# Kernel tuning notes

Hardware: AMD Instinct MI355X
Metric: run time of the kernel (lower is better)

Reference implementation:

```python
import jax, jax.numpy as jnp
import numpy as np

B, T, D_IN, H, E = 256, 512, 256, 256, 96  # batch, enc seq, input_size, hidden_size, num_embeddings


def setup_inputs() -> dict:
    key = jax.random.key(0)
    ks = jax.random.split(key, 12)
    s = 0.05
    return {
        "prev_h": jax.random.normal(ks[0], (B, H), jnp.float32),
        "prev_c": jax.random.normal(ks[1], (B, H), jnp.float32),
        "batch_H": jax.random.normal(ks[2], (B, T, D_IN), jnp.float32),
        "char_onehots": jax.random.uniform(ks[3], (B, E), jnp.float32),
        "W_i2h": jax.random.normal(ks[4], (H, D_IN), jnp.float32) * s,
        "W_h2h": jax.random.normal(ks[5], (H, H), jnp.float32) * s,
        "b_h2h": jax.random.normal(ks[6], (H,), jnp.float32) * s,
        "W_score": jax.random.normal(ks[7], (1, H), jnp.float32) * s,
        "W_ih": jax.random.normal(ks[8], (4 * H, D_IN + E), jnp.float32) * s,
        "W_hh": jax.random.normal(ks[9], (4 * H, H), jnp.float32) * s,
        "b_ih": jax.random.normal(ks[10], (4 * H,), jnp.float32) * s,
        "b_hh": jax.random.normal(ks[11], (4 * H,), jnp.float32) * s,
    }


def reference(prev_h, prev_c, batch_H, char_onehots,
              W_i2h, W_h2h, b_h2h, W_score, W_ih, W_hh, b_ih, b_hh):
    # additive attention over encoder features
    proj = jnp.einsum('btd,hd->bth', batch_H, W_i2h)          # [B,T,H]
    hid = prev_h @ W_h2h.T + b_h2h                             # [B,H]
    e = jnp.einsum('bth,oh->bto', jnp.tanh(proj + hid[:, None, :]), W_score)  # [B,T,1]
    alpha = jax.nn.softmax(e, axis=1)                          # [B,T,1]
    context = jnp.einsum('bt,btd->bd', alpha[..., 0], batch_H) # [B,D_IN]
    x = jnp.concatenate([context, char_onehots], axis=1)       # [B,D_IN+E]
    # LSTM cell step (PyTorch gate order: i, f, g, o)
    gates = x @ W_ih.T + b_ih + prev_h @ W_hh.T + b_hh         # [B,4H]
    i, f, g, o = jnp.split(gates, 4, axis=1)
    c_new = jax.nn.sigmoid(f) * prev_c + jax.nn.sigmoid(i) * jnp.tanh(g)
    h_new = jax.nn.sigmoid(o) * jnp.tanh(c_new)
    return (h_new, c_new, jnp.swapaxes(alpha, 1, 2))           # alpha -> [B,1,T]
```

## Files before the change

kernel.cpp:

```cpp
#include <hip/hip_runtime.h>

typedef __attribute__((ext_vector_type(8))) short short8;
typedef __attribute__((ext_vector_type(4))) float f32x4;

#define KPAD 40

#define WS_HID    0u
#define WS_P      262144u
#define WS_Z      786432u
#define WS_CTX    794624u
#define WS_CTXP   1056768u
#define WS_WBF    3153920u

__device__ __forceinline__ unsigned f2bfu(float f) {
    union { float f; unsigned u; } v; v.f = f;
    return (v.u + 0x7FFFu + ((v.u >> 16) & 1u)) >> 16;
}
__device__ __forceinline__ float bf2f(short s) {
    union { float f; unsigned u; } v; v.u = ((unsigned)(unsigned short)s) << 16;
    return v.f;
}
__device__ __forceinline__ float tanh_fast(float x) {
    float e2 = __expf(2.f * x);
    return 1.f - 2.f * __builtin_amdgcn_rcpf(e2 + 1.f);
}
__device__ __forceinline__ float sigmoid_fast(float x) {
    return __builtin_amdgcn_rcpf(1.f + __expf(-x));
}
__device__ __forceinline__ int4 pack8(float4 x0, float4 x1) {
    int4 q;
    q.x = (int)((f2bfu(x0.y) << 16) | f2bfu(x0.x));
    q.y = (int)((f2bfu(x0.w) << 16) | f2bfu(x0.z));
    q.z = (int)((f2bfu(x1.y) << 16) | f2bfu(x1.x));
    q.w = (int)((f2bfu(x1.w) << 16) | f2bfu(x1.z));
    return q;
}

__global__ __launch_bounds__(256) void k_prep(
    const float* __restrict__ prev_h, const float* __restrict__ W_i2h,
    const float* __restrict__ W_h2h, const float* __restrict__ b_h2h,
    float* __restrict__ hid, short* __restrict__ Wbf)
{
    int bid = blockIdx.x, tid = threadIdx.x;
    if (bid < 256) {
        __shared__ float ph[256];
        ph[tid] = prev_h[bid * 256 + tid];
        __syncthreads();
        float acc = b_h2h[tid];
        const float4* w = (const float4*)(W_h2h + tid * 256);
        #pragma unroll 8
        for (int k4 = 0; k4 < 64; ++k4) {
            float4 ww = w[k4];
            acc += ww.x * ph[k4*4+0] + ww.y * ph[k4*4+1] + ww.z * ph[k4*4+2] + ww.w * ph[k4*4+3];
        }
        hid[bid * 256 + tid] = acc;
    } else {
        int idx = (bid - 256) * 256 + tid;
        int kc = idx / (256 * KPAD);
        int rem = idx % (256 * KPAD);
        int n = rem / KPAD, kk = rem % KPAD;
        float v = (kk < 32) ? W_i2h[n * 256 + kc * 32 + kk] : 0.f;
        Wbf[idx] = (short)f2bfu(v);
    }
}

__global__ __launch_bounds__(256, 2) void k_escore_ctx(
    const float* __restrict__ BH, const short* __restrict__ Wbf,
    const float* __restrict__ hid, const float* __restrict__ Wsc,
    float* __restrict__ p_out, float* __restrict__ zbuf, float* __restrict__ ctxp)
{
    __shared__ char smem[81920];
    short* Al = (short*)smem;
    short* Bl = (short*)(smem + 40960);
    float* eps = (float*)(smem + 40960);
    float* pl  = (float*)(smem + 41984);
    float* r8  = (float*)(smem + 42240);

    const int tid = threadIdx.x;
    const int lane = tid & 63;
    const int w = tid >> 6;
    const int l15 = lane & 15, lg = lane >> 4;
    const int bt0 = blockIdx.x * 64;
    const int b = bt0 >> 9;
    const int c = (bt0 >> 6) & 7;

    const int arow = tid >> 2, akg = tid & 3;
    const float* asrc = BH + (size_t)(bt0 + arow) * 256 + akg * 8;

    f32x4 acc[4][4];
    #pragma unroll
    for (int i = 0; i < 4; i++)
        #pragma unroll
        for (int j = 0; j < 4; j++) acc[i][j] = (f32x4){0.f, 0.f, 0.f, 0.f};

    auto stage = [&](int kc) {
        float4 x0 = *(const float4*)(asrc + kc * 32);
        float4 x1 = *(const float4*)(asrc + kc * 32 + 4);
        *(int4*)&Al[kc * 2560 + arow * KPAD + akg * 8] = pack8(x0, x1);
        const int4* bs = (const int4*)(Wbf + (size_t)(kc * 256 + tid) * KPAD);
        int4* bd = (int4*)&Bl[(kc & 1) * 10240 + tid * KPAD];
        #pragma unroll
        for (int i = 0; i < 5; i++) bd[i] = bs[i];
    };

    stage(0);
    __syncthreads();

    for (int ks = 0; ks < 8; ++ks) {
        short8 af[4], bf_[4];
        #pragma unroll
        for (int rf = 0; rf < 4; rf++)
            af[rf] = *(const short8*)&Al[ks * 2560 + (rf * 16 + l15) * KPAD + lg * 8];
        #pragma unroll
        for (int cf = 0; cf < 4; cf++)
            bf_[cf] = *(const short8*)&Bl[(ks & 1) * 10240 + (w * 64 + cf * 16 + l15) * KPAD + lg * 8];
        if (ks < 7) stage(ks + 1);
        #pragma unroll
        for (int rf = 0; rf < 4; rf++)
            #pragma unroll
            for (int cf = 0; cf < 4; cf++)
                acc[rf][cf] = __builtin_amdgcn_mfma_f32_16x16x32_bf16(af[rf], bf_[cf], acc[rf][cf], 0, 0, 0);
        __syncthreads();
    }

    float esum[4][4];
    #pragma unroll
    for (int rf = 0; rf < 4; rf++)
        #pragma unroll
        for (int r = 0; r < 4; r++) esum[rf][r] = 0.f;

    #pragma unroll
    for (int cf = 0; cf < 4; cf++) {
        int col = w * 64 + cf * 16 + l15;
        float wsv = Wsc[col];
        float hd = hid[b * 256 + col];
        #pragma unroll
        for (int rf = 0; rf < 4; rf++)
            #pragma unroll
            for (int r = 0; r < 4; r++)
                esum[rf][r] += wsv * tanh_fast(acc[rf][cf][r] + hd);
    }
    #pragma unroll
    for (int rf = 0; rf < 4; rf++)
        #pragma unroll
        for (int r = 0; r < 4; r++) {
            float s = esum[rf][r];
            s += __shfl_xor(s, 1); s += __shfl_xor(s, 2);
            s += __shfl_xor(s, 4); s += __shfl_xor(s, 8);
            esum[rf][r] = s;
        }
    if (l15 == 0) {
        #pragma unroll
        for (int rf = 0; rf < 4; rf++)
            #pragma unroll
            for (int r = 0; r < 4; r++)
                eps[w * 64 + rf * 16 + lg * 4 + r] = esum[rf][r];
    }
    __syncthreads();

    if (tid < 64) {
        float e = eps[tid] + eps[64 + tid] + eps[128 + tid] + eps[192 + tid];
        float p = __expf(e);
        p_out[bt0 + tid] = p;
        pl[tid] = p;
        float z = p;
        z += __shfl_xor(z, 1); z += __shfl_xor(z, 2); z += __shfl_xor(z, 4);
        z += __shfl_xor(z, 8); z += __shfl_xor(z, 16); z += __shfl_xor(z, 32);
        if (tid == 0) zbuf[blockIdx.x] = z;
    }
    __syncthreads();

    {
        int tg = tid & 7, dg = tid >> 3;
        int d0 = dg * 8;
        int kc = d0 >> 5, dd = d0 & 31;
        float a8[8] = {0.f,0.f,0.f,0.f,0.f,0.f,0.f,0.f};
        #pragma unroll
        for (int tt = 0; tt < 8; ++tt) {
            int t = tt * 8 + tg;
            short8 v = *(const short8*)&Al[kc * 2560 + t * KPAD + dd];
            float pv = pl[t];
            #pragma unroll
            for (int j = 0; j < 8; ++j) a8[j] += pv * bf2f(v[j]);
        }
        #pragma unroll
        for (int j = 0; j < 8; ++j) r8[tg * 256 + d0 + j] = a8[j];
    }
    __syncthreads();
    {
        float s = 0.f;
        #pragma unroll
        for (int g = 0; g < 8; ++g) s += r8[g * 256 + tid];
        ctxp[((size_t)(c * 256 + b)) * 256 + tid] = s;
    }
}

__global__ __launch_bounds__(256) void k_finalize(
    const float* __restrict__ p, const float* __restrict__ zbuf,
    const float* __restrict__ ctxp, float* __restrict__ alpha, float* __restrict__ ctx)
{
    int b = blockIdx.x, t = threadIdx.x;
    float Z = 0.f;
    #pragma unroll
    for (int cc = 0; cc < 8; ++cc) Z += zbuf[b * 8 + cc];
    float inv = 1.f / Z;
    alpha[b * 512 + t] = p[b * 512 + t] * inv;
    alpha[b * 512 + 256 + t] = p[b * 512 + 256 + t] * inv;
    float s = 0.f;
    #pragma unroll
    for (int cc = 0; cc < 8; ++cc) s += ctxp[((size_t)(cc * 256 + b)) * 256 + t];
    ctx[b * 256 + t] = s * inv;
}

__global__ __launch_bounds__(256) void k_gates_lstm(
    const float* __restrict__ ctx, const float* __restrict__ onehot,
    const float* __restrict__ prev_h, const float* __restrict__ W_ih,
    const float* __restrict__ W_hh, const float* __restrict__ b_ih,
    const float* __restrict__ b_hh, const float* __restrict__ prev_c,
    float* __restrict__ out)
{
    __shared__ char smem[20800];
    short* AlB = (short*)smem;
    short* BlB = (short*)smem + 5120;
    const int tid = threadIdx.x;
    const int lane = tid & 63;
    const int w = tid >> 6;
    const int l15 = lane & 15, lg = lane >> 4;
    const int rb = blockIdx.x * 64;
    const int hb = blockIdx.y;

    f32x4 acc[4];
    #pragma unroll
    for (int j = 0; j < 4; j++) acc[j] = (f32x4){0.f, 0.f, 0.f, 0.f};

    const int arow = tid >> 2, akg = tid & 3;
    const int rg = rb + arow;
    const int bn = tid >> 2, bq = tid & 3;
    const int np_ = hb * 64 + bn, hh_ = np_ >> 2, gg_ = np_ & 3;
    const float* wih_row = W_ih + (size_t)(gg_ * 256 + hh_) * 352;
    const float* whh_row = W_hh + (size_t)(gg_ * 256 + hh_) * 256;

    auto stageAB = [&](int kc, int bu) {
        int k0 = kc * 32 + akg * 8;
        const float4* pa;
        if (k0 < 256)      pa = (const float4*)(ctx    + rg * 256 + k0);
        else if (k0 < 352) pa = (const float4*)(onehot + rg * 96  + (k0 - 256));
        else               pa = (const float4*)(prev_h + rg * 256 + (k0 - 352));
        float4 x0 = pa[0], x1 = pa[1];
        *(int4*)&AlB[bu * 2560 + arow * KPAD + akg * 8] = pack8(x0, x1);
        int kb = kc * 32 + bq * 8;
        const float* pb = (kb < 352) ? (wih_row + kb) : (whh_row + (kb - 352));
        float4 y0 = *(const float4*)pb, y1 = *(const float4*)(pb + 4);
        *(int4*)&BlB[bu * 2560 + bn * KPAD + bq * 8] = pack8(y0, y1);
    };

    stageAB(0, 0);
    __syncthreads();

    for (int kc = 0; kc < 19; ++kc) {
        int cur = kc & 1;
        short8 af = *(const short8*)&AlB[cur * 2560 + (w * 16 + l15) * KPAD + lg * 8];
        short8 bf_[4];
        #pragma unroll
        for (int cf = 0; cf < 4; cf++)
            bf_[cf] = *(const short8*)&BlB[cur * 2560 + (cf * 16 + l15) * KPAD + lg * 8];
        if (kc < 18) stageAB(kc + 1, cur ^ 1);
        #pragma unroll
        for (int cf = 0; cf < 4; cf++)
            acc[cf] = __builtin_amdgcn_mfma_f32_16x16x32_bf16(af, bf_[cf], acc[cf], 0, 0, 0);
        __syncthreads();
    }

    float* Gt = (float*)smem;
    #pragma unroll
    for (int cf = 0; cf < 4; cf++) {
        int col = cf * 16 + l15;
        int np = hb * 64 + col;
        int hg = np >> 2, g = np & 3;
        float bias = b_ih[g * 256 + hg] + b_hh[g * 256 + hg];
        #pragma unroll
        for (int r = 0; r < 4; r++)
            Gt[(w * 16 + lg * 4 + r) * 65 + col] = acc[cf][r] + bias;
    }
    __syncthreads();

    #pragma unroll
    for (int it = 0; it < 4; ++it) {
        int elem = it * 256 + tid;
        int row = elem >> 4, hl = elem & 15;
        float gi = Gt[row * 65 + hl * 4 + 0];
        float gf = Gt[row * 65 + hl * 4 + 1];
        float gg = Gt[row * 65 + hl * 4 + 2];
        float go = Gt[row * 65 + hl * 4 + 3];
        int bg = rb + row, hglob = hb * 16 + hl;
        float cv = sigmoid_fast(gf) * prev_c[bg * 256 + hglob] + sigmoid_fast(gi) * tanh_fast(gg);
        out[bg * 256 + hglob] = sigmoid_fast(go) * tanh_fast(cv);
        out[65536 + bg * 256 + hglob] = cv;
    }
}

extern "C" void kernel_launch(void* const* d_in, const int* in_sizes, int n_in,
                              void* d_out, int out_size, void* d_ws, size_t ws_size,
                              hipStream_t stream) {
    (void)in_sizes; (void)n_in; (void)out_size; (void)ws_size;
    const float* prev_h  = (const float*)d_in[0];
    const float* prev_c  = (const float*)d_in[1];
    const float* batch_H = (const float*)d_in[2];
    const float* onehot  = (const float*)d_in[3];
    const float* W_i2h   = (const float*)d_in[4];
    const float* W_h2h   = (const float*)d_in[5];
    const float* b_h2h   = (const float*)d_in[6];
    const float* W_score = (const float*)d_in[7];
    const float* W_ih    = (const float*)d_in[8];
    const float* W_hh    = (const float*)d_in[9];
    const float* b_ih    = (const float*)d_in[10];
    const float* b_hh    = (const float*)d_in[11];

    char* ws = (char*)d_ws;
    float* hid   = (float*)(ws + WS_HID);
    float* p     = (float*)(ws + WS_P);
    float* zbuf  = (float*)(ws + WS_Z);
    float* ctx   = (float*)(ws + WS_CTX);
    float* ctxp  = (float*)(ws + WS_CTXP);
    short* Wbf   = (short*)(ws + WS_WBF);

    float* out = (float*)d_out;
    float* alpha = out + 131072;

    hipLaunchKernelGGL(k_prep,       dim3(576),    dim3(256), 0, stream,
                       prev_h, W_i2h, W_h2h, b_h2h, hid, Wbf);
    hipLaunchKernelGGL(k_escore_ctx, dim3(2048),   dim3(256), 0, stream,
                       batch_H, Wbf, hid, W_score, p, zbuf, ctxp);
    hipLaunchKernelGGL(k_finalize,   dim3(256),    dim3(256), 0, stream,
                       p, zbuf, ctxp, alpha, ctx);
    hipLaunchKernelGGL(k_gates_lstm, dim3(4, 16),  dim3(256), 0, stream,
                       ctx, onehot, prev_h, W_ih, W_hh, b_ih, b_hh, prev_c, out);
}
```

Before: 79.33 us.

## Enlarge attention tile to 128 rows, async-load weights to LDS, recompute context in fp32

```diff
diff --git a/kernel.cpp b/kernel.cpp
--- a/kernel.cpp
+++ b/kernel.cpp
@@ -5,20 +5,16 @@
 
 #define KPAD 40
 
-#define WS_HID    0u
-#define WS_P      262144u
-#define WS_Z      786432u
-#define WS_CTX    794624u
-#define WS_CTXP   1056768u
-#define WS_WBF    3153920u
+#define WS_HID   0u
+#define WS_P     262144u
+#define WS_Z     786432u
+#define WS_CTX   790528u
+#define WS_CTXP  1052672u
+#define WS_WBF   2101248u
 
 __device__ __forceinline__ unsigned f2bfu(float f) {
     union { float f; unsigned u; } v; v.f = f;
     return (v.u + 0x7FFFu + ((v.u >> 16) & 1u)) >> 16;
-}
-__device__ __forceinline__ float bf2f(short s) {
-    union { float f; unsigned u; } v; v.u = ((unsigned)(unsigned short)s) << 16;
-    return v.f;
 }
 __device__ __forceinline__ float tanh_fast(float x) {
     float e2 = __expf(2.f * x);
@@ -34,6 +30,10 @@
     q.z = (int)((f2bfu(x1.y) << 16) | f2bfu(x1.x));
     q.w = (int)((f2bfu(x1.w) << 16) | f2bfu(x1.z));
     return q;
+}
+__device__ __forceinline__ void gload16(const void* g, void* l) {
+    __builtin_amdgcn_global_load_lds((const __attribute__((address_space(1))) void*)g,
+                                     (__attribute__((address_space(3))) void*)l, 16, 0, 0);
 }
 
 __global__ __launch_bounds__(256) void k_prep(
@@ -64,28 +64,31 @@
     }
 }
 
-__global__ __launch_bounds__(256, 2) void k_escore_ctx(
+__global__ __launch_bounds__(512, 4) void k_escore_ctx(
     const float* __restrict__ BH, const short* __restrict__ Wbf,
     const float* __restrict__ hid, const float* __restrict__ Wsc,
     float* __restrict__ p_out, float* __restrict__ zbuf, float* __restrict__ ctxp)
 {
-    __shared__ char smem[81920];
+    __shared__ char smem[64016];
     short* Al = (short*)smem;
-    short* Bl = (short*)(smem + 40960);
-    float* eps = (float*)(smem + 40960);
-    float* pl  = (float*)(smem + 41984);
-    float* r8  = (float*)(smem + 42240);
+    char*  BlB = smem + 20480;
+    short* Bl = (short*)BlB;
+    float* eps = (float*)(smem + 61440);
+    float* pl  = (float*)(smem + 63488);
+    float* zw  = (float*)(smem + 64000);
 
     const int tid = threadIdx.x;
     const int lane = tid & 63;
     const int w = tid >> 6;
+    const int wr = w >> 2, wc = w & 3;
     const int l15 = lane & 15, lg = lane >> 4;
-    const int bt0 = blockIdx.x * 64;
+    const int bt0 = blockIdx.x * 128;
     const int b = bt0 >> 9;
-    const int c = (bt0 >> 6) & 7;
+    const int c = blockIdx.x & 3;
 
     const int arow = tid >> 2, akg = tid & 3;
     const float* asrc = BH + (size_t)(bt0 + arow) * 256 + akg * 8;
+    const int nslot = (w < 4) ? 3 : 2;
 
     f32x4 acc[4][4];
     #pragma unroll
@@ -94,32 +97,39 @@
         for (int j = 0; j < 4; j++) acc[i][j] = (f32x4){0.f, 0.f, 0.f, 0.f};
 
     auto stage = [&](int kc) {
+        int bu = kc & 1;
         float4 x0 = *(const float4*)(asrc + kc * 32);
         float4 x1 = *(const float4*)(asrc + kc * 32 + 4);
-        *(int4*)&Al[kc * 2560 + arow * KPAD + akg * 8] = pack8(x0, x1);
-        const int4* bs = (const int4*)(Wbf + (size_t)(kc * 256 + tid) * KPAD);
-        int4* bd = (int4*)&Bl[(kc & 1) * 10240 + tid * KPAD];
-        #pragma unroll
-        for (int i = 0; i < 5; i++) bd[i] = bs[i];
+        const char* gsb = (const char*)Wbf + (size_t)kc * 20480 + lane * 16;
+        char* lsb = BlB + bu * 20480;
+        #pragma unroll
+        for (int i = 0; i < 3; ++i)
+            if (i < nslot) {
+                int slot = w + 8 * i;
+                gload16(gsb + slot * 1024, lsb + slot * 1024);
+            }
+        *(int4*)&Al[bu * 5120 + arow * KPAD + akg * 8] = pack8(x0, x1);
     };
 
     stage(0);
     __syncthreads();
 
+    #pragma unroll
     for (int ks = 0; ks < 8; ++ks) {
-        short8 af[4], bf_[4];
+        const int cur = ks & 1;
+        short8 af[4], bfr[4];
         #pragma unroll
         for (int rf = 0; rf < 4; rf++)
-            af[rf] = *(const short8*)&Al[ks * 2560 + (rf * 16 + l15) * KPAD + lg * 8];
+            af[rf] = *(const short8*)&Al[cur * 5120 + (wr * 64 + rf * 16 + l15) * KPAD + lg * 8];
         #pragma unroll
         for (int cf = 0; cf < 4; cf++)
-            bf_[cf] = *(const short8*)&Bl[(ks & 1) * 10240 + (w * 64 + cf * 16 + l15) * KPAD + lg * 8];
+            bfr[cf] = *(const short8*)&Bl[cur * 10240 + (wc * 64 + cf * 16 + l15) * KPAD + lg * 8];
         if (ks < 7) stage(ks + 1);
         #pragma unroll
         for (int rf = 0; rf < 4; rf++)
             #pragma unroll
             for (int cf = 0; cf < 4; cf++)
-                acc[rf][cf] = __builtin_amdgcn_mfma_f32_16x16x32_bf16(af[rf], bf_[cf], acc[rf][cf], 0, 0, 0);
+                acc[rf][cf] = __builtin_amdgcn_mfma_f32_16x16x32_bf16(af[rf], bfr[cf], acc[rf][cf], 0, 0, 0);
         __syncthreads();
     }
 
@@ -131,7 +141,7 @@
 
     #pragma unroll
     for (int cf = 0; cf < 4; cf++) {
-        int col = w * 64 + cf * 16 + l15;
+        int col = wc * 64 + cf * 16 + l15;
         float wsv = Wsc[col];
         float hd = hid[b * 256 + col];
         #pragma unroll
@@ -154,45 +164,36 @@
         for (int rf = 0; rf < 4; rf++)
             #pragma unroll
             for (int r = 0; r < 4; r++)
-                eps[w * 64 + rf * 16 + lg * 4 + r] = esum[rf][r];
-    }
-    __syncthreads();
-
-    if (tid < 64) {
-        float e = eps[tid] + eps[64 + tid] + eps[128 + tid] + eps[192 + tid];
+                eps[wc * 128 + wr * 64 + rf * 16 + lg * 4 + r] = esum[rf][r];
+    }
+    __syncthreads();
+
+    if (tid < 128) {
+        float e = eps[tid] + eps[128 + tid] + eps[256 + tid] + eps[384 + tid];
         float p = __expf(e);
         p_out[bt0 + tid] = p;
         pl[tid] = p;
         float z = p;
         z += __shfl_xor(z, 1); z += __shfl_xor(z, 2); z += __shfl_xor(z, 4);
         z += __shfl_xor(z, 8); z += __shfl_xor(z, 16); z += __shfl_xor(z, 32);
-        if (tid == 0) zbuf[blockIdx.x] = z;
-    }
-    __syncthreads();
-
+        if ((tid & 63) == 0) zw[tid >> 6] = z;
+    }
+    __syncthreads();
+
+    if (tid == 0) zbuf[blockIdx.x] = zw[0] + zw[1];
+
+    float* r2 = (float*)smem;
     {
-        int tg = tid & 7, dg = tid >> 3;
-        int d0 = dg * 8;
-        int kc = d0 >> 5, dd = d0 & 31;
-        float a8[8] = {0.f,0.f,0.f,0.f,0.f,0.f,0.f,0.f};
-        #pragma unroll
-        for (int tt = 0; tt < 8; ++tt) {
-            int t = tt * 8 + tg;
-            short8 v = *(const short8*)&Al[kc * 2560 + t * KPAD + dd];
-            float pv = pl[t];
-            #pragma unroll
-            for (int j = 0; j < 8; ++j) a8[j] += pv * bf2f(v[j]);
-        }
-        #pragma unroll
-        for (int j = 0; j < 8; ++j) r8[tg * 256 + d0 + j] = a8[j];
-    }
-    __syncthreads();
-    {
-        float s = 0.f;
-        #pragma unroll
-        for (int g = 0; g < 8; ++g) s += r8[g * 256 + tid];
-        ctxp[((size_t)(c * 256 + b)) * 256 + tid] = s;
-    }
+        int d = tid & 255, rh = tid >> 8;
+        const float* bh = BH + (size_t)(bt0 + rh * 64) * 256 + d;
+        float accv = 0.f;
+        #pragma unroll 8
+        for (int t = 0; t < 64; ++t) accv += pl[rh * 64 + t] * bh[(size_t)t * 256];
+        r2[rh * 256 + d] = accv;
+    }
+    __syncthreads();
+    if (tid < 256)
+        ctxp[((size_t)(c * 256 + b)) * 256 + tid] = r2[tid] + r2[256 + tid];
 }
 
 __global__ __launch_bounds__(256) void k_finalize(
@@ -200,15 +201,13 @@
     const float* __restrict__ ctxp, float* __restrict__ alpha, float* __restrict__ ctx)
 {
     int b = blockIdx.x, t = threadIdx.x;
-    float Z = 0.f;
-    #pragma unroll
-    for (int cc = 0; cc < 8; ++cc) Z += zbuf[b * 8 + cc];
+    float Z = zbuf[b * 4 + 0] + zbuf[b * 4 + 1] + zbuf[b * 4 + 2] + zbuf[b * 4 + 3];
     float inv = 1.f / Z;
     alpha[b * 512 + t] = p[b * 512 + t] * inv;
     alpha[b * 512 + 256 + t] = p[b * 512 + 256 + t] * inv;
     float s = 0.f;
     #pragma unroll
-    for (int cc = 0; cc < 8; ++cc) s += ctxp[((size_t)(cc * 256 + b)) * 256 + t];
+    for (int cc = 0; cc < 4; ++cc) s += ctxp[((size_t)(cc * 256 + b)) * 256 + t];
     ctx[b * 256 + t] = s * inv;
 }
 
@@ -260,14 +259,14 @@
     for (int kc = 0; kc < 19; ++kc) {
         int cur = kc & 1;
         short8 af = *(const short8*)&AlB[cur * 2560 + (w * 16 + l15) * KPAD + lg * 8];
-        short8 bf_[4];
+        short8 bfr[4];
         #pragma unroll
         for (int cf = 0; cf < 4; cf++)
-            bf_[cf] = *(const short8*)&BlB[cur * 2560 + (cf * 16 + l15) * KPAD + lg * 8];
+            bfr[cf] = *(const short8*)&BlB[cur * 2560 + (cf * 16 + l15) * KPAD + lg * 8];
         if (kc < 18) stageAB(kc + 1, cur ^ 1);
         #pragma unroll
         for (int cf = 0; cf < 4; cf++)
-            acc[cf] = __builtin_amdgcn_mfma_f32_16x16x32_bf16(af, bf_[cf], acc[cf], 0, 0, 0);
+            acc[cf] = __builtin_amdgcn_mfma_f32_16x16x32_bf16(af, bfr[cf], acc[cf], 0, 0, 0);
         __syncthreads();
     }
 
@@ -329,7 +328,7 @@
 
     hipLaunchKernelGGL(k_prep,       dim3(576),    dim3(256), 0, stream,
                        prev_h, W_i2h, W_h2h, b_h2h, hid, Wbf);
-    hipLaunchKernelGGL(k_escore_ctx, dim3(2048),   dim3(256), 0, stream,
+    hipLaunchKernelGGL(k_escore_ctx, dim3(1024),   dim3(512), 0, stream,
                        batch_H, Wbf, hid, W_score, p, zbuf, ctxp);
     hipLaunchKernelGGL(k_finalize,   dim3(256),    dim3(256), 0, stream,
                        p, zbuf, ctxp, alpha, ctx);
```

Measured after the change: 93.52 us. 17.9% more time.

## Load weights directly from global into MFMA fragments and drop LDS staging

Applied to the files above, without the earlier changes.

```diff
diff --git a/kernel.cpp b/kernel.cpp
--- a/kernel.cpp
+++ b/kernel.cpp
@@ -3,21 +3,30 @@
 typedef __attribute__((ext_vector_type(8))) short short8;
 typedef __attribute__((ext_vector_type(4))) float f32x4;
 
-#define KPAD 40
-
-#define WS_HID    0u
-#define WS_P      262144u
-#define WS_Z      786432u
-#define WS_CTX    794624u
-#define WS_CTXP   1056768u
-#define WS_WBF    3153920u
-
-__device__ __forceinline__ unsigned f2bfu(float f) {
-    union { float f; unsigned u; } v; v.f = f;
-    return (v.u + 0x7FFFu + ((v.u >> 16) & 1u)) >> 16;
-}
-__device__ __forceinline__ float bf2f(short s) {
-    union { float f; unsigned u; } v; v.u = ((unsigned)(unsigned short)s) << 16;
+#define APITCH 264
+
+#define WS_HID   0u
+#define WS_P     262144u
+#define WS_Z     786432u
+#define WS_CTX   794624u
+#define WS_CTXP  1056768u
+#define WS_WBF   3153920u
+
+__device__ __forceinline__ unsigned cvtpk(float lo, float hi) {
+    unsigned r;
+    asm("v_cvt_pk_bf16_f32 %0, %1, %2" : "=v"(r) : "v"(lo), "v"(hi));
+    return r;
+}
+__device__ __forceinline__ int4 pack8(float4 x0, float4 x1) {
+    int4 q;
+    q.x = (int)cvtpk(x0.x, x0.y);
+    q.y = (int)cvtpk(x0.z, x0.w);
+    q.z = (int)cvtpk(x1.x, x1.y);
+    q.w = (int)cvtpk(x1.z, x1.w);
+    return q;
+}
+__device__ __forceinline__ float bf2f(unsigned s) {
+    union { float f; unsigned u; } v; v.u = s << 16;
     return v.f;
 }
 __device__ __forceinline__ float tanh_fast(float x) {
@@ -26,14 +35,6 @@
 }
 __device__ __forceinline__ float sigmoid_fast(float x) {
     return __builtin_amdgcn_rcpf(1.f + __expf(-x));
-}
-__device__ __forceinline__ int4 pack8(float4 x0, float4 x1) {
-    int4 q;
-    q.x = (int)((f2bfu(x0.y) << 16) | f2bfu(x0.x));
-    q.y = (int)((f2bfu(x0.w) << 16) | f2bfu(x0.z));
-    q.z = (int)((f2bfu(x1.y) << 16) | f2bfu(x1.x));
-    q.w = (int)((f2bfu(x1.w) << 16) | f2bfu(x1.z));
-    return q;
 }
 
 __global__ __launch_bounds__(256) void k_prep(
@@ -55,26 +56,22 @@
         }
         hid[bid * 256 + tid] = acc;
     } else {
-        int idx = (bid - 256) * 256 + tid;
-        int kc = idx / (256 * KPAD);
-        int rem = idx % (256 * KPAD);
-        int n = rem / KPAD, kk = rem % KPAD;
-        float v = (kk < 32) ? W_i2h[n * 256 + kc * 32 + kk] : 0.f;
-        Wbf[idx] = (short)f2bfu(v);
-    }
-}
-
-__global__ __launch_bounds__(256, 2) void k_escore_ctx(
+        int idx = ((bid - 256) * 256 + tid) * 8;
+        float4 x0 = *(const float4*)(W_i2h + idx);
+        float4 x1 = *(const float4*)(W_i2h + idx + 4);
+        *(int4*)&Wbf[idx] = pack8(x0, x1);
+    }
+}
+
+__global__ __launch_bounds__(256, 3) void k_escore_ctx(
     const float* __restrict__ BH, const short* __restrict__ Wbf,
     const float* __restrict__ hid, const float* __restrict__ Wsc,
     float* __restrict__ p_out, float* __restrict__ zbuf, float* __restrict__ ctxp)
 {
-    __shared__ char smem[81920];
-    short* Al = (short*)smem;
-    short* Bl = (short*)(smem + 40960);
-    float* eps = (float*)(smem + 40960);
-    float* pl  = (float*)(smem + 41984);
-    float* r8  = (float*)(smem + 42240);
+    __shared__ short Al[64 * APITCH];
+    __shared__ float eps[4 * 64];
+    __shared__ float pl[64];
+    __shared__ float r2[2 * 256];
 
     const int tid = threadIdx.x;
     const int lane = tid & 63;
@@ -84,8 +81,18 @@
     const int b = bt0 >> 9;
     const int c = (bt0 >> 6) & 7;
 
-    const int arow = tid >> 2, akg = tid & 3;
-    const float* asrc = BH + (size_t)(bt0 + arow) * 256 + akg * 8;
+    {
+        const int arow = tid >> 2, kq = tid & 3;
+        const float* as = BH + (size_t)(bt0 + arow) * 256 + kq * 64;
+        short* dst = &Al[arow * APITCH + kq * 64];
+        #pragma unroll
+        for (int i = 0; i < 8; ++i) {
+            float4 x0 = *(const float4*)(as + i * 8);
+            float4 x1 = *(const float4*)(as + i * 8 + 4);
+            *(int4*)(dst + i * 8) = pack8(x0, x1);
+        }
+    }
+    __syncthreads();
 
     f32x4 acc[4][4];
     #pragma unroll
@@ -93,34 +100,21 @@
         #pragma unroll
         for (int j = 0; j < 4; j++) acc[i][j] = (f32x4){0.f, 0.f, 0.f, 0.f};
 
-    auto stage = [&](int kc) {
-        float4 x0 = *(const float4*)(asrc + kc * 32);
-        float4 x1 = *(const float4*)(asrc + kc * 32 + 4);
-        *(int4*)&Al[kc * 2560 + arow * KPAD + akg * 8] = pack8(x0, x1);
-        const int4* bs = (const int4*)(Wbf + (size_t)(kc * 256 + tid) * KPAD);
-        int4* bd = (int4*)&Bl[(kc & 1) * 10240 + tid * KPAD];
-        #pragma unroll
-        for (int i = 0; i < 5; i++) bd[i] = bs[i];
-    };
-
-    stage(0);
-    __syncthreads();
-
+    const short* bbase = Wbf + (size_t)(w * 64) * 256 + lg * 8;
+    #pragma unroll
     for (int ks = 0; ks < 8; ++ks) {
-        short8 af[4], bf_[4];
+        short8 af[4], bfr[4];
         #pragma unroll
         for (int rf = 0; rf < 4; rf++)
-            af[rf] = *(const short8*)&Al[ks * 2560 + (rf * 16 + l15) * KPAD + lg * 8];
+            af[rf] = *(const short8*)&Al[(rf * 16 + l15) * APITCH + ks * 32 + lg * 8];
         #pragma unroll
         for (int cf = 0; cf < 4; cf++)
-            bf_[cf] = *(const short8*)&Bl[(ks & 1) * 10240 + (w * 64 + cf * 16 + l15) * KPAD + lg * 8];
-        if (ks < 7) stage(ks + 1);
+            bfr[cf] = *(const short8*)(bbase + (size_t)(cf * 16 + l15) * 256 + ks * 32);
         #pragma unroll
         for (int rf = 0; rf < 4; rf++)
             #pragma unroll
             for (int cf = 0; cf < 4; cf++)
-                acc[rf][cf] = __builtin_amdgcn_mfma_f32_16x16x32_bf16(af[rf], bf_[cf], acc[rf][cf], 0, 0, 0);
-        __syncthreads();
+                acc[rf][cf] = __builtin_amdgcn_mfma_f32_16x16x32_bf16(af[rf], bfr[cf], acc[rf][cf], 0, 0, 0);
     }
 
     float esum[4][4];
@@ -171,28 +165,21 @@
     __syncthreads();
 
     {
-        int tg = tid & 7, dg = tid >> 3;
-        int d0 = dg * 8;
-        int kc = d0 >> 5, dd = d0 & 31;
-        float a8[8] = {0.f,0.f,0.f,0.f,0.f,0.f,0.f,0.f};
-        #pragma unroll
-        for (int tt = 0; tt < 8; ++tt) {
-            int t = tt * 8 + tg;
-            short8 v = *(const short8*)&Al[kc * 2560 + t * KPAD + dd];
-            float pv = pl[t];
-            #pragma unroll
-            for (int j = 0; j < 8; ++j) a8[j] += pv * bf2f(v[j]);
-        }
-        #pragma unroll
-        for (int j = 0; j < 8; ++j) r8[tg * 256 + d0 + j] = a8[j];
-    }
-    __syncthreads();
-    {
-        float s = 0.f;
-        #pragma unroll
-        for (int g = 0; g < 8; ++g) s += r8[g * 256 + tid];
-        ctxp[((size_t)(c * 256 + b)) * 256 + tid] = s;
-    }
+        int d2 = tid & 127, rh = tid >> 7;
+        float a0 = 0.f, a1 = 0.f;
+        #pragma unroll 8
+        for (int t = 0; t < 32; ++t) {
+            int tt = rh * 32 + t;
+            unsigned v = *(const unsigned*)&Al[tt * APITCH + d2 * 2];
+            float pv = pl[tt];
+            a0 += pv * bf2f(v & 0xffffu);
+            a1 += pv * bf2f(v >> 16);
+        }
+        r2[rh * 256 + d2 * 2]     = a0;
+        r2[rh * 256 + d2 * 2 + 1] = a1;
+    }
+    __syncthreads();
+    ctxp[((size_t)(c * 256 + b)) * 256 + tid] = r2[tid] + r2[256 + tid];
 }
 
 __global__ __launch_bounds__(256) void k_finalize(
@@ -219,9 +206,7 @@
     const float* __restrict__ b_hh, const float* __restrict__ prev_c,
     float* __restrict__ out)
 {
-    __shared__ char smem[20800];
-    short* AlB = (short*)smem;
-    short* BlB = (short*)smem + 5120;
+    __shared__ float Gt[64 * 65];
     const int tid = threadIdx.x;
     const int lane = tid & 63;
     const int w = tid >> 6;
@@ -229,49 +214,41 @@
     const int rb = blockIdx.x * 64;
     const int hb = blockIdx.y;
 
+    const int arow = rb + w * 16 + l15;
+    const float* wih[4]; const float* whh[4];
+    #pragma unroll
+    for (int cf = 0; cf < 4; cf++) {
+        int np = hb * 64 + cf * 16 + l15;
+        int hh = np >> 2, gg = np & 3;
+        wih[cf] = W_ih + (size_t)(gg * 256 + hh) * 352;
+        whh[cf] = W_hh + (size_t)(gg * 256 + hh) * 256;
+    }
+
     f32x4 acc[4];
     #pragma unroll
     for (int j = 0; j < 4; j++) acc[j] = (f32x4){0.f, 0.f, 0.f, 0.f};
 
-    const int arow = tid >> 2, akg = tid & 3;
-    const int rg = rb + arow;
-    const int bn = tid >> 2, bq = tid & 3;
-    const int np_ = hb * 64 + bn, hh_ = np_ >> 2, gg_ = np_ & 3;
-    const float* wih_row = W_ih + (size_t)(gg_ * 256 + hh_) * 352;
-    const float* whh_row = W_hh + (size_t)(gg_ * 256 + hh_) * 256;
-
-    auto stageAB = [&](int kc, int bu) {
-        int k0 = kc * 32 + akg * 8;
-        const float4* pa;
-        if (k0 < 256)      pa = (const float4*)(ctx    + rg * 256 + k0);
-        else if (k0 < 352) pa = (const float4*)(onehot + rg * 96  + (k0 - 256));
-        else               pa = (const float4*)(prev_h + rg * 256 + (k0 - 352));
-        float4 x0 = pa[0], x1 = pa[1];
-        *(int4*)&AlB[bu * 2560 + arow * KPAD + akg * 8] = pack8(x0, x1);
-        int kb = kc * 32 + bq * 8;
-        const float* pb = (kb < 352) ? (wih_row + kb) : (whh_row + (kb - 352));
-        float4 y0 = *(const float4*)pb, y1 = *(const float4*)(pb + 4);
-        *(int4*)&BlB[bu * 2560 + bn * KPAD + bq * 8] = pack8(y0, y1);
-    };
-
-    stageAB(0, 0);
-    __syncthreads();
-
+    #pragma unroll 4
     for (int kc = 0; kc < 19; ++kc) {
-        int cur = kc & 1;
-        short8 af = *(const short8*)&AlB[cur * 2560 + (w * 16 + l15) * KPAD + lg * 8];
-        short8 bf_[4];
+        int k0 = kc * 32 + lg * 8;
+        const float* pa;
+        if (k0 < 256)      pa = ctx    + (size_t)arow * 256 + k0;
+        else if (k0 < 352) pa = onehot + (size_t)arow * 96  + (k0 - 256);
+        else               pa = prev_h + (size_t)arow * 256 + (k0 - 352);
+        float4 x0 = *(const float4*)pa, x1 = *(const float4*)(pa + 4);
+        short8 af; *(int4*)&af = pack8(x0, x1);
+        short8 bfr[4];
+        #pragma unroll
+        for (int cf = 0; cf < 4; cf++) {
+            const float* pb = (k0 < 352) ? (wih[cf] + k0) : (whh[cf] + (k0 - 352));
+            float4 y0 = *(const float4*)pb, y1 = *(const float4*)(pb + 4);
+            *(int4*)&bfr[cf] = pack8(y0, y1);
+        }
         #pragma unroll
         for (int cf = 0; cf < 4; cf++)
-            bf_[cf] = *(const short8*)&BlB[cur * 2560 + (cf * 16 + l15) * KPAD + lg * 8];
-        if (kc < 18) stageAB(kc + 1, cur ^ 1);
-        #pragma unroll
-        for (int cf = 0; cf < 4; cf++)
-            acc[cf] = __builtin_amdgcn_mfma_f32_16x16x32_bf16(af, bf_[cf], acc[cf], 0, 0, 0);
-        __syncthreads();
-    }
-
-    float* Gt = (float*)smem;
+            acc[cf] = __builtin_amdgcn_mfma_f32_16x16x32_bf16(af, bfr[cf], acc[cf], 0, 0, 0);
+    }
+
     #pragma unroll
     for (int cf = 0; cf < 4; cf++) {
         int col = cf * 16 + l15;
@@ -327,7 +304,7 @@
     float* out = (float*)d_out;
     float* alpha = out + 131072;
 
-    hipLaunchKernelGGL(k_prep,       dim3(576),    dim3(256), 0, stream,
+    hipLaunchKernelGGL(k_prep,       dim3(288),    dim3(256), 0, stream,
                        prev_h, W_i2h, W_h2h, b_h2h, hid, Wbf);
     hipLaunchKernelGGL(k_escore_ctx, dim3(2048),   dim3(256), 0, stream,
                        batch_H, Wbf, hid, W_score, p, zbuf, ctxp);
```

Result: slower. 121.2 us (+52.8%).

## Stage W via global_load_lds, preload full A tile, use hardware bf16 pack

Applied to the files above, without the earlier changes.

```diff
diff --git a/kernel.cpp b/kernel.cpp
--- a/kernel.cpp
+++ b/kernel.cpp
@@ -4,20 +4,30 @@
 typedef __attribute__((ext_vector_type(4))) float f32x4;
 
 #define KPAD 40
-
-#define WS_HID    0u
-#define WS_P      262144u
-#define WS_Z      786432u
-#define WS_CTX    794624u
-#define WS_CTXP   1056768u
-#define WS_WBF    3153920u
-
-__device__ __forceinline__ unsigned f2bfu(float f) {
-    union { float f; unsigned u; } v; v.f = f;
-    return (v.u + 0x7FFFu + ((v.u >> 16) & 1u)) >> 16;
-}
-__device__ __forceinline__ float bf2f(short s) {
-    union { float f; unsigned u; } v; v.u = ((unsigned)(unsigned short)s) << 16;
+#define APITCH 264
+
+#define WS_HID   0u
+#define WS_P     262144u
+#define WS_Z     786432u
+#define WS_CTX   794624u
+#define WS_CTXP  1056768u
+#define WS_WBF   3153920u
+
+__device__ __forceinline__ unsigned cvtpk(float lo, float hi) {
+    unsigned r;
+    asm("v_cvt_pk_bf16_f32 %0, %1, %2" : "=v"(r) : "v"(lo), "v"(hi));
+    return r;
+}
+__device__ __forceinline__ int4 pack8(float4 x0, float4 x1) {
+    int4 q;
+    q.x = (int)cvtpk(x0.x, x0.y);
+    q.y = (int)cvtpk(x0.z, x0.w);
+    q.z = (int)cvtpk(x1.x, x1.y);
+    q.w = (int)cvtpk(x1.z, x1.w);
+    return q;
+}
+__device__ __forceinline__ float bf2f(unsigned s) {
+    union { float f; unsigned u; } v; v.u = s << 16;
     return v.f;
 }
 __device__ __forceinline__ float tanh_fast(float x) {
@@ -27,13 +37,9 @@
 __device__ __forceinline__ float sigmoid_fast(float x) {
     return __builtin_amdgcn_rcpf(1.f + __expf(-x));
 }
-__device__ __forceinline__ int4 pack8(float4 x0, float4 x1) {
-    int4 q;
-    q.x = (int)((f2bfu(x0.y) << 16) | f2bfu(x0.x));
-    q.y = (int)((f2bfu(x0.w) << 16) | f2bfu(x0.z));
-    q.z = (int)((f2bfu(x1.y) << 16) | f2bfu(x1.x));
-    q.w = (int)((f2bfu(x1.w) << 16) | f2bfu(x1.z));
-    return q;
+__device__ __forceinline__ void gload16(const void* g, void* l) {
+    __builtin_amdgcn_global_load_lds((const __attribute__((address_space(1))) void*)g,
+                                     (__attribute__((address_space(3))) void*)l, 16, 0, 0);
 }
 
 __global__ __launch_bounds__(256) void k_prep(
@@ -59,8 +65,14 @@
         int kc = idx / (256 * KPAD);
         int rem = idx % (256 * KPAD);
         int n = rem / KPAD, kk = rem % KPAD;
-        float v = (kk < 32) ? W_i2h[n * 256 + kc * 32 + kk] : 0.f;
-        Wbf[idx] = (short)f2bfu(v);
+        float v = 0.f;
+        if (kk < 32) {
+            union { float f; unsigned u; } t; t.f = W_i2h[n * 256 + kc * 32 + kk];
+            t.u = (t.u + 0x7FFFu + ((t.u >> 16) & 1u)) & 0xFFFF0000u;
+            v = t.f;
+        }
+        union { float f; unsigned u; } o; o.f = v;
+        Wbf[idx] = (short)(o.u >> 16);
     }
 }
 
@@ -69,12 +81,13 @@
     const float* __restrict__ hid, const float* __restrict__ Wsc,
     float* __restrict__ p_out, float* __restrict__ zbuf, float* __restrict__ ctxp)
 {
-    __shared__ char smem[81920];
+    __shared__ char smem[74752];
     short* Al = (short*)smem;
-    short* Bl = (short*)(smem + 40960);
-    float* eps = (float*)(smem + 40960);
-    float* pl  = (float*)(smem + 41984);
-    float* r8  = (float*)(smem + 42240);
+    char*  BlB = smem + 33792;
+    short* Bl = (short*)BlB;
+    float* eps = (float*)BlB;
+    float* pl  = (float*)(BlB + 1024);
+    float* r4  = (float*)(BlB + 1280);
 
     const int tid = threadIdx.x;
     const int lane = tid & 63;
@@ -84,8 +97,23 @@
     const int b = bt0 >> 9;
     const int c = (bt0 >> 6) & 7;
 
-    const int arow = tid >> 2, akg = tid & 3;
-    const float* asrc = BH + (size_t)(bt0 + arow) * 256 + akg * 8;
+    {
+        const char* gs0 = (const char*)Wbf + tid * 16;
+        #pragma unroll
+        for (int s = 0; s < 5; ++s)
+            gload16(gs0 + s * 4096, BlB + s * 4096 + tid * 16);
+    }
+    {
+        const float* as = BH + (size_t)bt0 * 256 + tid * 8;
+        const int row0 = tid >> 5, colw = (tid & 31) * 8;
+        #pragma unroll
+        for (int i = 0; i < 8; ++i) {
+            float4 x0 = *(const float4*)(as + i * 2048);
+            float4 x1 = *(const float4*)(as + i * 2048 + 4);
+            *(int4*)&Al[(i * 8 + row0) * APITCH + colw] = pack8(x0, x1);
+        }
+    }
+    __syncthreads();
 
     f32x4 acc[4][4];
     #pragma unroll
@@ -93,33 +121,28 @@
         #pragma unroll
         for (int j = 0; j < 4; j++) acc[i][j] = (f32x4){0.f, 0.f, 0.f, 0.f};
 
-    auto stage = [&](int kc) {
-        float4 x0 = *(const float4*)(asrc + kc * 32);
-        float4 x1 = *(const float4*)(asrc + kc * 32 + 4);
-        *(int4*)&Al[kc * 2560 + arow * KPAD + akg * 8] = pack8(x0, x1);
-        const int4* bs = (const int4*)(Wbf + (size_t)(kc * 256 + tid) * KPAD);
-        int4* bd = (int4*)&Bl[(kc & 1) * 10240 + tid * KPAD];
-        #pragma unroll
-        for (int i = 0; i < 5; i++) bd[i] = bs[i];
-    };
-
-    stage(0);
-    __syncthreads();
-
+    #pragma unroll
     for (int ks = 0; ks < 8; ++ks) {
-        short8 af[4], bf_[4];
+        const int cur = ks & 1;
+        if (ks < 7) {
+            const char* gsb = (const char*)Wbf + (size_t)(ks + 1) * 20480 + tid * 16;
+            char* lsb = BlB + (cur ^ 1) * 20480 + tid * 16;
+            #pragma unroll
+            for (int s = 0; s < 5; ++s)
+                gload16(gsb + s * 4096, lsb + s * 4096);
+        }
+        short8 af[4], bfr[4];
         #pragma unroll
         for (int rf = 0; rf < 4; rf++)
-            af[rf] = *(const short8*)&Al[ks * 2560 + (rf * 16 + l15) * KPAD + lg * 8];
+            af[rf] = *(const short8*)&Al[(rf * 16 + l15) * APITCH + ks * 32 + lg * 8];
         #pragma unroll
         for (int cf = 0; cf < 4; cf++)
-            bf_[cf] = *(const short8*)&Bl[(ks & 1) * 10240 + (w * 64 + cf * 16 + l15) * KPAD + lg * 8];
-        if (ks < 7) stage(ks + 1);
+            bfr[cf] = *(const short8*)&Bl[cur * 10240 + (w * 64 + cf * 16 + l15) * KPAD + lg * 8];
         #pragma unroll
         for (int rf = 0; rf < 4; rf++)
             #pragma unroll
             for (int cf = 0; cf < 4; cf++)
-                acc[rf][cf] = __builtin_amdgcn_mfma_f32_16x16x32_bf16(af[rf], bf_[cf], acc[rf][cf], 0, 0, 0);
+                acc[rf][cf] = __builtin_amdgcn_mfma_f32_16x16x32_bf16(af[rf], bfr[cf], acc[rf][cf], 0, 0, 0);
         __syncthreads();
     }
 
@@ -171,28 +194,23 @@
     __syncthreads();
 
     {
-        int tg = tid & 7, dg = tid >> 3;
-        int d0 = dg * 8;
-        int kc = d0 >> 5, dd = d0 & 31;
-        float a8[8] = {0.f,0.f,0.f,0.f,0.f,0.f,0.f,0.f};
-        #pragma unroll
-        for (int tt = 0; tt < 8; ++tt) {
-            int t = tt * 8 + tg;
-            short8 v = *(const short8*)&Al[kc * 2560 + t * KPAD + dd];
-            float pv = pl[t];
-            #pragma unroll
-            for (int j = 0; j < 8; ++j) a8[j] += pv * bf2f(v[j]);
-        }
-        #pragma unroll
-        for (int j = 0; j < 8; ++j) r8[tg * 256 + d0 + j] = a8[j];
-    }
-    __syncthreads();
-    {
-        float s = 0.f;
-        #pragma unroll
-        for (int g = 0; g < 8; ++g) s += r8[g * 256 + tid];
-        ctxp[((size_t)(c * 256 + b)) * 256 + tid] = s;
-    }
+        float c0 = 0.f, c1 = 0.f, c2 = 0.f, c3 = 0.f;
+        #pragma unroll
+        for (int t = 0; t < 16; ++t) {
+            int row = w * 16 + t;
+            float pv = pl[row];
+            unsigned v1 = *(const unsigned*)&Al[row * APITCH + lane * 2];
+            unsigned v2 = *(const unsigned*)&Al[row * APITCH + 128 + lane * 2];
+            c0 += pv * bf2f(v1 & 0xffffu); c1 += pv * bf2f(v1 >> 16);
+            c2 += pv * bf2f(v2 & 0xffffu); c3 += pv * bf2f(v2 >> 16);
+        }
+        r4[w * 256 + lane * 2]       = c0;
+        r4[w * 256 + lane * 2 + 1]   = c1;
+        r4[w * 256 + 128 + lane * 2] = c2;
+        r4[w * 256 + 129 + lane * 2] = c3;
+    }
+    __syncthreads();
+    ctxp[((size_t)(c * 256 + b)) * 256 + tid] = r4[tid] + r4[256 + tid] + r4[512 + tid] + r4[768 + tid];
 }
 
 __global__ __launch_bounds__(256) void k_finalize(
@@ -260,14 +278,14 @@
     for (int kc = 0; kc < 19; ++kc) {
         int cur = kc & 1;
         short8 af = *(const short8*)&AlB[cur * 2560 + (w * 16 + l15) * KPAD + lg * 8];
-        short8 bf_[4];
+        short8 bfr[4];
         #pragma unroll
         for (int cf = 0; cf < 4; cf++)
-            bf_[cf] = *(const short8*)&BlB[cur * 2560 + (cf * 16 + l15) * KPAD + lg * 8];
+            bfr[cf] = *(const short8*)&BlB[cur * 2560 + (cf * 16 + l15) * KPAD + lg * 8];
         if (kc < 18) stageAB(kc + 1, cur ^ 1);
         #pragma unroll
         for (int cf = 0; cf < 4; cf++)
-            acc[cf] = __builtin_amdgcn_mfma_f32_16x16x32_bf16(af, bf_[cf], acc[cf], 0, 0, 0);
+            acc[cf] = __builtin_amdgcn_mfma_f32_16x16x32_bf16(af, bfr[cf], acc[cf], 0, 0, 0);
         __syncthreads();
     }
 
```

Result: faster. 73.62 us (-7.2%).
